# Kernel tuning notes

Hardware: AMD Instinct MI355X
Metric: run time of the kernel (lower is better)

The kernel has to match this reference:

```python
import jax, jax.numpy as jnp
import numpy as np

DIM = 768
HEAD = 12


def setup_inputs() -> dict:
    key = jax.random.key(0)
    ks = jax.random.split(key, 7)
    B, N, C = 4, 2048, DIM
    s = 0.02
    return {
        "x": jax.random.normal(ks[0], (B, N, C), dtype=jnp.float32),
        "wq": jax.random.normal(ks[1], (C, C), dtype=jnp.float32) * s,
        "bq": jax.random.normal(ks[2], (C,), dtype=jnp.float32) * s,
        "wkv": jax.random.normal(ks[3], (C, 2 * C), dtype=jnp.float32) * s,
        "bkv": jax.random.normal(ks[4], (2 * C,), dtype=jnp.float32) * s,
        "wp": jax.random.normal(ks[5], (C, C), dtype=jnp.float32) * s,
        "bp": jax.random.normal(ks[6], (C,), dtype=jnp.float32) * s,
    }


def reference(x, wq, bq, wkv, bkv, wp, bp):
    B, N, C = x.shape
    H = HEAD
    D = C // H
    scale = D ** -0.5
    # projections
    q = (x @ wq + bq).reshape(B, N, H, D)          # [B,N,H,D]
    kv = (x @ wkv + bkv).reshape(B, N, 2, H, D)
    k = kv[:, :, 0]                                 # [B,N,H,D]
    v = kv[:, :, 1]
    # attention scores [B,H,N,N]
    attn = jnp.einsum('bnhd,bmhd->bhnm', q, k) * scale
    attn = jax.nn.softmax(attn, axis=-1)
    x_atten = jnp.einsum('bhnm,bmhd->bnhd', attn, v).reshape(B, N, C)
    return x_atten @ wp + bp
```

## Files before the change

### kernel.cpp

```cpp
#include <hip/hip_runtime.h>

typedef unsigned short u16;
typedef __attribute__((ext_vector_type(8))) short bf16x8;
typedef __attribute__((ext_vector_type(4))) float f32x4;

#define MFMA(a, b, c) __builtin_amdgcn_mfma_f32_16x16x32_bf16(a, b, c, 0, 0, 0)
#define LOG2E 1.44269504088896340736f

__device__ __forceinline__ u16 f2bf(float f) {
    union { float f; unsigned u; } v; v.f = f;
    unsigned r = v.u + 0x7fffu + ((v.u >> 16) & 1u);
    return (u16)(r >> 16);
}
__device__ __forceinline__ float bf2f(u16 h) {
    union { unsigned u; float f; } v; v.u = ((unsigned)h) << 16;
    return v.f;
}
__device__ __forceinline__ unsigned pkbf(float a, float b) {
#if __has_builtin(__builtin_amdgcn_cvt_pk_bf16_f32)
    typedef __attribute__((ext_vector_type(2))) __bf16 bf2_t;
    bf2_t v = __builtin_amdgcn_cvt_pk_bf16_f32(a, b);
    return __builtin_bit_cast(unsigned, v);
#else
    return (unsigned)f2bf(a) | ((unsigned)f2bf(b) << 16);
#endif
}
__device__ __forceinline__ float ex2(float x) {
#if __has_builtin(__builtin_amdgcn_exp2f)
    return __builtin_amdgcn_exp2f(x);
#else
    return exp2f(x);
#endif
}
__device__ __forceinline__ bf16x8 frag_from(unsigned a, unsigned b, unsigned c, unsigned d) {
    uint4 v; v.x = a; v.y = b; v.z = c; v.w = d;
    return __builtin_bit_cast(bf16x8, v);
}

__device__ __forceinline__ void g2l16(const void* g, void* lds_base) {
    __builtin_amdgcn_global_load_lds(
        (const __attribute__((address_space(1))) unsigned*)(unsigned long long)(uintptr_t)g,
        (__attribute__((address_space(3))) unsigned*)(unsigned)(uintptr_t)lds_base,
        16, 0, 0);
}

__global__ void cvt_kernel(const float* __restrict__ in, u16* __restrict__ out, int n) {
    int i = (blockIdx.x * 256 + threadIdx.x) * 4;
    if (i >= n) return;
    float4 v = *(const float4*)&in[i];
    uint2 o;
    o.x = pkbf(v.x, v.y);
    o.y = pkbf(v.z, v.w);
    *(uint2*)&out[i] = o;
}

__global__ void transpose_cvt3(const float* __restrict__ wq, const float* __restrict__ wkv,
                               const float* __restrict__ wp,
                               u16* __restrict__ wtqkv, u16* __restrict__ wtp) {
    __shared__ float tile[32][33];
    const float* W; u16* Wt; int cols;
    if (blockIdx.z == 0)      { W = wq;  Wt = wtqkv;             cols = 768; }
    else if (blockIdx.z == 1) { W = wkv; Wt = wtqkv + 768 * 768; cols = 1536; }
    else                      { W = wp;  Wt = wtp;               cols = 768; }
    int bx = blockIdx.x * 32, by = blockIdx.y * 32;
    if (bx >= cols) return;
    int tx = threadIdx.x, ty = threadIdx.y;
    for (int i = 0; i < 4; i++)
        tile[ty + 8 * i][tx] = W[(size_t)(by + ty + 8 * i) * cols + bx + tx];
    __syncthreads();
    for (int i = 0; i < 4; i++)
        Wt[(size_t)(bx + ty + 8 * i) * 768 + by + tx] = f2bf(tile[tx][ty + 8 * i]);
}

__global__ __launch_bounds__(256) void vt_kernel(const u16* __restrict__ qkv,
                                                 u16* __restrict__ vtg) {
    __shared__ unsigned tile[64 * 65];
    int t = threadIdx.x;
    int h = blockIdx.y, b = blockIdx.z, kt = blockIdx.x * 64;
    int kr = t >> 2, dch = (t & 3) * 16;
    const u16* src = &qkv[(size_t)(b * 2048 + kt + kr) * 2304 + 1536 + h * 64 + dch];
    bf16x8 v0 = *(const bf16x8*)src;
    bf16x8 v1 = *(const bf16x8*)(src + 8);
    for (int j = 0; j < 8; j++) {
        tile[kr * 65 + dch + j]     = (u16)v0[j];
        tile[kr * 65 + dch + 8 + j] = (u16)v1[j];
    }
    __syncthreads();
    for (int rnd = 0; rnd < 2; rnd++) {
        int d = rnd * 32 + (t >> 3);
        int m = t & 7;
        int k0 = 32 * (m >> 2) + 4 * (m & 3);
        uint4 o;
        o.x = tile[(k0 + 0) * 65 + d]  | (tile[(k0 + 1) * 65 + d]  << 16);
        o.y = tile[(k0 + 2) * 65 + d]  | (tile[(k0 + 3) * 65 + d]  << 16);
        o.z = tile[(k0 + 16) * 65 + d] | (tile[(k0 + 17) * 65 + d] << 16);
        o.w = tile[(k0 + 18) * 65 + d] | (tile[(k0 + 19) * 65 + d] << 16);
        *(uint4*)&vtg[((size_t)(b * 12 + h) * 64 + d) * 2048 + kt + m * 8] = o;
    }
}

__global__ __launch_bounds__(256, 3) void gemm128(
    const u16* __restrict__ A, const u16* __restrict__ Bt,
    const float* __restrict__ bias0, const float* __restrict__ bias1, int bsplit,
    u16* __restrict__ outB, int M, int N, int K)
{
    __shared__ __align__(16) u16 smem[17408];
    u16* As = smem;
    u16* Bs = smem + 8192;
    u16* Cs = smem;

    int t = threadIdx.x;
    int w = t >> 6, l = t & 63, q4 = l >> 4, lm = l & 15, lm7 = l & 7;
    int bm = blockIdx.y * 128, bn = blockIdx.x * 128;
    int wm = (w >> 1) * 64, wn = (w & 1) * 64;

    f32x4 acc[4][4];
    for (int i = 0; i < 4; i++) for (int j = 0; j < 4; j++) acc[i][j] = (f32x4){0, 0, 0, 0};

    int srow = l >> 3;
    int schunk = (l & 7) ^ srow;

    for (int kt = 0; kt < K; kt += 64) {
        for (int p = 0; p < 4; p++) {
            int row = p * 32 + w * 8 + srow;
            g2l16(&A [(size_t)(bm + row) * K + kt + schunk * 8], &As[(p * 32 + w * 8) * 64]);
            g2l16(&Bt[(size_t)(bn + row) * K + kt + schunk * 8], &Bs[(p * 32 + w * 8) * 64]);
        }
        __syncthreads();
        bf16x8 a[4][2], b[4][2];
        for (int i = 0; i < 4; i++)
            for (int kc = 0; kc < 2; kc++) {
                a[i][kc] = *(const bf16x8*)&As[(wm + 16 * i + lm) * 64 + ((4 * kc + q4) ^ lm7) * 8];
                b[i][kc] = *(const bf16x8*)&Bs[(wn + 16 * i + lm) * 64 + ((4 * kc + q4) ^ lm7) * 8];
            }
        for (int kc = 0; kc < 2; kc++)
            for (int i = 0; i < 4; i++)
                for (int j = 0; j < 4; j++)
                    acc[i][j] = MFMA(a[i][kc], b[j][kc], acc[i][j]);
        __syncthreads();
    }

    for (int i = 0; i < 4; i++)
        for (int j = 0; j < 4; j++) {
            int col = bn + wn + 16 * j + lm;
            float bv = (col < bsplit) ? bias0[col] : bias1[col - bsplit];
            for (int r = 0; r < 4; r++)
                Cs[(wm + 16 * i + 4 * q4 + r) * 132 + wn + 16 * j + lm] =
                    f2bf(acc[i][j][r] + bv);
        }
    __syncthreads();
    int row = t >> 1, c0 = (t & 1) * 8;
    for (int s = 0; s < 8; s++)
        *(uint4*)&outB[(size_t)(bm + row) * N + bn + c0 + s * 16] =
            *(const uint4*)&Cs[row * 132 + c0 + s * 16];
}

__global__ __launch_bounds__(256, 4) void gemm_n64(
    const u16* __restrict__ A, const u16* __restrict__ Bt,
    const float* __restrict__ bias, float* __restrict__ outF, int M, int N, int K)
{
    __shared__ __align__(16) u16 smem[12288];
    u16* As = smem;
    u16* Bs = smem + 8192;

    int t = threadIdx.x;
    int w = t >> 6, l = t & 63, q4 = l >> 4, lm = l & 15, lm7 = l & 7;
    int bm = blockIdx.y * 128, bn = blockIdx.x * 64;
    int wm = (w >> 1) * 64, wn = (w & 1) * 32;

    f32x4 acc[4][2];
    for (int i = 0; i < 4; i++) for (int j = 0; j < 2; j++) acc[i][j] = (f32x4){0, 0, 0, 0};

    int srow = l >> 3;
    int schunk = (l & 7) ^ srow;

    for (int kt = 0; kt < K; kt += 64) {
        for (int p = 0; p < 4; p++) {
            int row = p * 32 + w * 8 + srow;
            g2l16(&A[(size_t)(bm + row) * K + kt + schunk * 8], &As[(p * 32 + w * 8) * 64]);
        }
        for (int p = 0; p < 2; p++) {
            int row = p * 32 + w * 8 + srow;
            g2l16(&Bt[(size_t)(bn + row) * K + kt + schunk * 8], &Bs[(p * 32 + w * 8) * 64]);
        }
        __syncthreads();
        bf16x8 a[4][2], b[2][2];
        for (int i = 0; i < 4; i++)
            for (int kc = 0; kc < 2; kc++)
                a[i][kc] = *(const bf16x8*)&As[(wm + 16 * i + lm) * 64 + ((4 * kc + q4) ^ lm7) * 8];
        for (int j = 0; j < 2; j++)
            for (int kc = 0; kc < 2; kc++)
                b[j][kc] = *(const bf16x8*)&Bs[(wn + 16 * j + lm) * 64 + ((4 * kc + q4) ^ lm7) * 8];
        for (int kc = 0; kc < 2; kc++)
            for (int i = 0; i < 4; i++)
                for (int j = 0; j < 2; j++)
                    acc[i][j] = MFMA(a[i][kc], b[j][kc], acc[i][j]);
        __syncthreads();
    }

    for (int i = 0; i < 4; i++)
        for (int j = 0; j < 2; j++) {
            int col = bn + wn + 16 * j + lm;
            float bv = bias[col];
            for (int r = 0; r < 4; r++) {
                int row = bm + wm + 16 * i + 4 * q4 + r;
                outF[(size_t)row * N + col] = acc[i][j][r] + bv;
            }
        }
}

__global__ __launch_bounds__(256, 3) void attn_kernel(const u16* __restrict__ qkv,
                                                      const u16* __restrict__ vtg,
                                                      u16* __restrict__ xatt)
{
    __shared__ __align__(16) u16 smem[16384];

    int t = threadIdx.x;
    int w = t >> 6, l = t & 63, q4 = l >> 4, lm = l & 15, lm7 = l & 7;
    int h = blockIdx.y, b = blockIdx.z;
    int qw = blockIdx.x * 128 + w * 32;
    size_t rowbase = (size_t)b * 2048;
    int bh = b * 12 + h;

    int srow = l >> 3;
    int schunk = (l & 7) ^ srow;
    const u16* ksrc[2];
    const u16* vsrc[2];
    for (int p = 0; p < 2; p++) {
        int row = w * 16 + p * 8 + srow;
        ksrc[p] = &qkv[(rowbase + row) * 2304 + 768 + h * 64 + schunk * 8];
        vsrc[p] = &vtg[((size_t)bh * 64 + row) * 2048 + schunk * 8];
    }

    bf16x8 qf[2][2];
    for (int qi = 0; qi < 2; qi++) {
        size_t row = rowbase + qw + 16 * qi + lm;
        for (int kq = 0; kq < 2; kq++) {
            bf16x8 raw = *(const bf16x8*)&qkv[row * 2304 + h * 64 + kq * 32 + q4 * 8];
            bf16x8 sc;
            for (int j = 0; j < 8; j++) sc[j] = (short)f2bf(bf2f((u16)raw[j]) * (0.125f * LOG2E));
            qf[qi][kq] = sc;
        }
    }

    int offA = lm * 64 + (q4 ^ lm7) * 8;
    int offB = lm * 64 + ((4 | q4) ^ lm7) * 8;

    float lst[2] = {0.f, 0.f};
    f32x4 acc[2][4];
    for (int qi = 0; qi < 2; qi++)
        for (int dt = 0; dt < 4; dt++) acc[qi][dt] = (f32x4){0, 0, 0, 0};

    for (int p = 0; p < 2; p++) {
        g2l16(ksrc[p], smem + (w * 16 + p * 8) * 64);
        g2l16(vsrc[p], smem + 8192 + (w * 16 + p * 8) * 64);
    }

    for (int it = 0; it < 32; it++) {
        __syncthreads();
        int buf = it & 1;
        if (it + 1 < 32) {
            int nbuf = buf ^ 1;
            for (int p = 0; p < 2; p++) {
                g2l16(ksrc[p] + (size_t)(it + 1) * 64 * 2304,
                      smem + nbuf * 4096 + (w * 16 + p * 8) * 64);
                g2l16(vsrc[p] + (it + 1) * 64,
                      smem + 8192 + nbuf * 4096 + (w * 16 + p * 8) * 64);
            }
        }
        const u16* Kb = smem + buf * 4096;
        const u16* Vb = smem + 8192 + buf * 4096;

        f32x4 s[2][4];
        for (int kt2 = 0; kt2 < 4; kt2++) {
            bf16x8 kf0 = *(const bf16x8*)&Kb[kt2 * 1024 + offA];
            bf16x8 kf1 = *(const bf16x8*)&Kb[kt2 * 1024 + offB];
            for (int qi = 0; qi < 2; qi++) {
                f32x4 z = {0, 0, 0, 0};
                z = MFMA(kf0, qf[qi][0], z);
                z = MFMA(kf1, qf[qi][1], z);
                s[qi][kt2] = z;
            }
        }

        bf16x8 vf0[4], vf1[4];
        for (int dt = 0; dt < 4; dt++) {
            vf0[dt] = *(const bf16x8*)&Vb[dt * 1024 + offA];
            vf1[dt] = *(const bf16x8*)&Vb[dt * 1024 + offB];
        }

        for (int qi = 0; qi < 2; qi++) {
            float su = 0.f;
            uint2 pk[4];
            for (int kt2 = 0; kt2 < 4; kt2++) {
                float p0 = ex2(s[qi][kt2][0]);
                float p1 = ex2(s[qi][kt2][1]);
                float p2 = ex2(s[qi][kt2][2]);
                float p3 = ex2(s[qi][kt2][3]);
                su += (p0 + p1) + (p2 + p3);
                pk[kt2].x = pkbf(p0, p1);
                pk[kt2].y = pkbf(p2, p3);
            }
            su += __shfl_xor(su, 16);
            su += __shfl_xor(su, 32);
            lst[qi] += su;

            bf16x8 af0 = frag_from(pk[0].x, pk[0].y, pk[1].x, pk[1].y);
            bf16x8 af1 = frag_from(pk[2].x, pk[2].y, pk[3].x, pk[3].y);
            for (int dt = 0; dt < 4; dt++) {
                acc[qi][dt] = MFMA(af0, vf0[dt], acc[qi][dt]);
                acc[qi][dt] = MFMA(af1, vf1[dt], acc[qi][dt]);
            }
        }
    }

    for (int qi = 0; qi < 2; qi++) {
        float linv = 1.0f / lst[qi];
        float ar[4];
        for (int r = 0; r < 4; r++) ar[r] = __shfl(linv, 4 * q4 + r);
        for (int dt = 0; dt < 4; dt++)
            for (int r = 0; r < 4; r++) {
                int row = qw + 16 * qi + 4 * q4 + r;
                xatt[(rowbase + row) * 768 + h * 64 + 16 * dt + lm] =
                    f2bf(acc[qi][dt][r] * ar[r]);
            }
    }
}

extern "C" void kernel_launch(void* const* d_in, const int* in_sizes, int n_in,
                              void* d_out, int out_size, void* d_ws, size_t ws_size,
                              hipStream_t stream)
{
    const float* x   = (const float*)d_in[0];
    const float* wq  = (const float*)d_in[1];
    const float* bq  = (const float*)d_in[2];
    const float* wkv = (const float*)d_in[3];
    const float* bkv = (const float*)d_in[4];
    const float* wp  = (const float*)d_in[5];
    const float* bp  = (const float*)d_in[6];
    float* out = (float*)d_out;

    char* ws = (char*)d_ws;
    u16* xb    = (u16*)(ws);
    u16* wtqkv = (u16*)(ws + 12582912);
    u16* wtp   = (u16*)(ws + 16121856);
    u16* qkvb  = (u16*)(ws + 17301504);
    u16* xatt  = (u16*)(ws + 55050240);
    u16* vtg   = xb;

    cvt_kernel<<<6144, 256, 0, stream>>>(x, xb, 8192 * 768);
    transpose_cvt3<<<dim3(48, 24, 3), dim3(32, 8), 0, stream>>>(wq, wkv, wp, wtqkv, wtp);

    gemm128<<<dim3(2304 / 128, 8192 / 128), 256, 0, stream>>>(
        xb, wtqkv, bq, bkv, 768, qkvb, 8192, 2304, 768);

    vt_kernel<<<dim3(32, 12, 4), 256, 0, stream>>>(qkvb, vtg);

    attn_kernel<<<dim3(16, 12, 4), 256, 0, stream>>>(qkvb, vtg, xatt);

    gemm_n64<<<dim3(768 / 64, 8192 / 128), 256, 0, stream>>>(
        xatt, wtp, bp, out, 8192, 768, 768);
}
```

Baseline: 232.8 us.

## Fuse input/weight conversion kernels and write transposed V from QKV GEMM epilogue

Merges the x bf16 conversion and the weight transpose-convert into a single prep kernel launch. It also removes the separate V-transpose kernel: the QKV GEMM epilogue writes V tiles directly in transposed [b,h,d,n] layout into a new workspace region. This saves two launches and a full read/write pass over V. The cost is a strided LDS gather in the GEMM epilogue, and workspace must be large enough for the new vtg offset.

```diff
diff --git a/kernel.cpp b/kernel.cpp
--- a/kernel.cpp
+++ b/kernel.cpp
@@ -44,27 +44,30 @@
         16, 0, 0);
 }
 
-__global__ void cvt_kernel(const float* __restrict__ in, u16* __restrict__ out, int n) {
-    int i = (blockIdx.x * 256 + threadIdx.x) * 4;
-    if (i >= n) return;
-    float4 v = *(const float4*)&in[i];
-    uint2 o;
-    o.x = pkbf(v.x, v.y);
-    o.y = pkbf(v.z, v.w);
-    *(uint2*)&out[i] = o;
-}
-
-__global__ void transpose_cvt3(const float* __restrict__ wq, const float* __restrict__ wkv,
-                               const float* __restrict__ wp,
-                               u16* __restrict__ wtqkv, u16* __restrict__ wtp) {
+__global__ __launch_bounds__(256) void prep_kernel(
+    const float* __restrict__ x, const float* __restrict__ wq,
+    const float* __restrict__ wkv, const float* __restrict__ wp,
+    u16* __restrict__ xb, u16* __restrict__ wtqkv, u16* __restrict__ wtp)
+{
+    int bz = blockIdx.x;
+    int t = threadIdx.x;
+    if (bz < 6144) {
+        int i = (bz * 256 + t) * 4;
+        float4 v = *(const float4*)&x[i];
+        uint2 o;
+        o.x = pkbf(v.x, v.y);
+        o.y = pkbf(v.z, v.w);
+        *(uint2*)&xb[i] = o;
+        return;
+    }
     __shared__ float tile[32][33];
-    const float* W; u16* Wt; int cols;
-    if (blockIdx.z == 0)      { W = wq;  Wt = wtqkv;             cols = 768; }
-    else if (blockIdx.z == 1) { W = wkv; Wt = wtqkv + 768 * 768; cols = 1536; }
-    else                      { W = wp;  Wt = wtp;               cols = 768; }
-    int bx = blockIdx.x * 32, by = blockIdx.y * 32;
-    if (bx >= cols) return;
-    int tx = threadIdx.x, ty = threadIdx.y;
+    const float* W; u16* Wt; int cols; int r = bz - 6144;
+    if (r < 576)       { W = wq;  Wt = wtqkv;             cols = 768;  }
+    else if (r < 1728) { W = wkv; Wt = wtqkv + 768 * 768; cols = 1536; r -= 576; }
+    else               { W = wp;  Wt = wtp;               cols = 768;  r -= 1728; }
+    int nbx = cols / 32;
+    int bx = (r % nbx) * 32, by = (r / nbx) * 32;
+    int tx = t & 31, ty = t >> 5;
     for (int i = 0; i < 4; i++)
         tile[ty + 8 * i][tx] = W[(size_t)(by + ty + 8 * i) * cols + bx + tx];
     __syncthreads();
@@ -72,37 +75,10 @@
         Wt[(size_t)(bx + ty + 8 * i) * 768 + by + tx] = f2bf(tile[tx][ty + 8 * i]);
 }
 
-__global__ __launch_bounds__(256) void vt_kernel(const u16* __restrict__ qkv,
-                                                 u16* __restrict__ vtg) {
-    __shared__ unsigned tile[64 * 65];
-    int t = threadIdx.x;
-    int h = blockIdx.y, b = blockIdx.z, kt = blockIdx.x * 64;
-    int kr = t >> 2, dch = (t & 3) * 16;
-    const u16* src = &qkv[(size_t)(b * 2048 + kt + kr) * 2304 + 1536 + h * 64 + dch];
-    bf16x8 v0 = *(const bf16x8*)src;
-    bf16x8 v1 = *(const bf16x8*)(src + 8);
-    for (int j = 0; j < 8; j++) {
-        tile[kr * 65 + dch + j]     = (u16)v0[j];
-        tile[kr * 65 + dch + 8 + j] = (u16)v1[j];
-    }
-    __syncthreads();
-    for (int rnd = 0; rnd < 2; rnd++) {
-        int d = rnd * 32 + (t >> 3);
-        int m = t & 7;
-        int k0 = 32 * (m >> 2) + 4 * (m & 3);
-        uint4 o;
-        o.x = tile[(k0 + 0) * 65 + d]  | (tile[(k0 + 1) * 65 + d]  << 16);
-        o.y = tile[(k0 + 2) * 65 + d]  | (tile[(k0 + 3) * 65 + d]  << 16);
-        o.z = tile[(k0 + 16) * 65 + d] | (tile[(k0 + 17) * 65 + d] << 16);
-        o.w = tile[(k0 + 18) * 65 + d] | (tile[(k0 + 19) * 65 + d] << 16);
-        *(uint4*)&vtg[((size_t)(b * 12 + h) * 64 + d) * 2048 + kt + m * 8] = o;
-    }
-}
-
 __global__ __launch_bounds__(256, 3) void gemm128(
     const u16* __restrict__ A, const u16* __restrict__ Bt,
     const float* __restrict__ bias0, const float* __restrict__ bias1, int bsplit,
-    u16* __restrict__ outB, int M, int N, int K)
+    u16* __restrict__ outB, u16* __restrict__ vtg, int M, int N, int K)
 {
     __shared__ __align__(16) u16 smem[17408];
     u16* As = smem;
@@ -149,10 +125,29 @@
                     f2bf(acc[i][j][r] + bv);
         }
     __syncthreads();
-    int row = t >> 1, c0 = (t & 1) * 8;
-    for (int s = 0; s < 8; s++)
-        *(uint4*)&outB[(size_t)(bm + row) * N + bn + c0 + s * 16] =
-            *(const uint4*)&Cs[row * 132 + c0 + s * 16];
+
+    if (bn < 1536) {
+        int row = t >> 1, c0 = (t & 1) * 8;
+        for (int s = 0; s < 8; s++)
+            *(uint4*)&outB[(size_t)(bm + row) * N + bn + c0 + s * 16] =
+                *(const uint4*)&Cs[row * 132 + c0 + s * 16];
+    } else {
+        int c = t >> 1, half = t & 1;
+        int d = c & 63, hloc = c >> 6;
+        int b = bm >> 11;
+        int bh = b * 12 + ((bn - 1536) >> 6) + hloc;
+        size_t rowoff = ((size_t)bh * 64 + d) * 2048 + (bm & 2047) + half * 64;
+        const u16* base = &Cs[c];
+        for (int oct = 0; oct < 8; oct++) {
+            int n0 = 32 * (2 * half + (oct >> 2)) + 4 * (oct & 3);
+            uint4 o;
+            o.x = base[(n0 + 0)  * 132] | ((unsigned)base[(n0 + 1)  * 132] << 16);
+            o.y = base[(n0 + 2)  * 132] | ((unsigned)base[(n0 + 3)  * 132] << 16);
+            o.z = base[(n0 + 16) * 132] | ((unsigned)base[(n0 + 17) * 132] << 16);
+            o.w = base[(n0 + 18) * 132] | ((unsigned)base[(n0 + 19) * 132] << 16);
+            *(uint4*)&vtg[rowoff + oct * 8] = o;
+        }
+    }
 }
 
 __global__ __launch_bounds__(256, 4) void gemm_n64(
@@ -346,15 +341,12 @@
     u16* wtp   = (u16*)(ws + 16121856);
     u16* qkvb  = (u16*)(ws + 17301504);
     u16* xatt  = (u16*)(ws + 55050240);
-    u16* vtg   = xb;
-
-    cvt_kernel<<<6144, 256, 0, stream>>>(x, xb, 8192 * 768);
-    transpose_cvt3<<<dim3(48, 24, 3), dim3(32, 8), 0, stream>>>(wq, wkv, wp, wtqkv, wtp);
+    u16* vtg   = (u16*)(ws + 67632128);
+
+    prep_kernel<<<8448, 256, 0, stream>>>(x, wq, wkv, wp, xb, wtqkv, wtp);
 
     gemm128<<<dim3(2304 / 128, 8192 / 128), 256, 0, stream>>>(
-        xb, wtqkv, bq, bkv, 768, qkvb, 8192, 2304, 768);
-
-    vt_kernel<<<dim3(32, 12, 4), 256, 0, stream>>>(qkvb, vtg);
+        xb, wtqkv, bq, bkv, 768, qkvb, vtg, 8192, 2304, 768);
 
     attn_kernel<<<dim3(16, 12, 4), 256, 0, stream>>>(qkvb, vtg, xatt);
 
```

Result: faster. 221.6 us (-4.8%).
